# Performance work log

Hardware: AMD Instinct MI355X
Metric: run time of the kernel (lower is better)

Reference implementation:

```python
import jax, jax.numpy as jnp
import numpy as np

BATCH = 256
DIMS = [256, 512, 256, 128]  # input_dim + hidden_dims + [output_dim]
GRID = 5


def _kan_layer(x, w, s, b, g):
    # x: (B, in); w: (out, in, G); s: (out, in); b: (out,); g: (G,)
    xn = jnp.tanh(x)
    # distances: (B, out, in, G)
    d = jnp.abs(xn[:, None, :, None] - g[None, None, None, :])
    basis = jnp.exp(-d * s[None, :, :, None])
    # sum over grid then in_features, fused into one einsum
    return jnp.einsum('boig,oig->bo', basis, w) + b


def setup_inputs() -> dict:
    key = jax.random.key(0)
    ks = jax.random.split(key, 8)
    inp = {'x': jax.random.normal(ks[0], (BATCH, DIMS[0]), dtype=jnp.float32)}
    for i in range(3):
        din, dout = DIMS[i], DIMS[i + 1]
        k1, k2 = jax.random.split(ks[i + 1])
        inp[f'w{i}'] = jax.random.normal(k1, (dout, din, GRID), dtype=jnp.float32)
        inp[f's{i}'] = jax.random.normal(k2, (dout, din), dtype=jnp.float32)
        inp[f'b{i}'] = jnp.zeros((dout,), dtype=jnp.float32)
        inp[f'g{i}'] = jnp.linspace(-1.0, 1.0, GRID, dtype=jnp.float32)
    return inp


def reference(x, w0, s0, b0, g0, w1, s1, b1, g1, w2, s2, b2, g2):
    h = _kan_layer(x, w0, s0, b0, g0)
    h = jax.nn.relu(h)
    h = _kan_layer(h, w1, s1, b1, g1)
    h = jax.nn.relu(h)
    h = _kan_layer(h, w2, s2, b2, g2)
    return jnp.tanh(h)
```

## Files before the change

### kernel.cpp

```cpp
#include <hip/hip_runtime.h>
#include <math.h>

#define BATCH 256
#define D0 256
#define D1 512
#define D2 256
#define D3 128

__device__ float g_xnT0[D0 * BATCH];
__device__ float g_xnT1[D1 * BATCH];
__device__ float g_xnT2[D2 * BATCH];

template <int L> __device__ __forceinline__ float* xnT_ptr() {
    if constexpr (L == 0) return g_xnT0;
    else if constexpr (L == 1) return g_xnT1;
    else return g_xnT2;
}

__device__ __forceinline__ float tanh_f32_cr(float x) {
    return (float)tanh((double)x);
}

__global__ void prep_tanhT(const float* __restrict__ x) {
    int i = threadIdx.x;
    int b = blockIdx.x;
    g_xnT0[i * BATCH + b] = tanh_f32_cr(x[b * D0 + i]);
}

template <int IN, int LU>
__device__ __forceinline__ float sse_chain(const float* __restrict__ xnT,
                                           const float* __restrict__ wr,
                                           const float* __restrict__ sr,
                                           const int b)
{
#pragma clang fp contract(off)
    constexpr int K = IN * 5;
    float acc = 0.f;

#pragma unroll 1
    for (int blk = 0; blk < K; blk += 80) {
        const int ibase = blk / 5;
        float xnv[16], svv[16];
#pragma unroll
        for (int ii = 0; ii < 16; ++ii) {
            xnv[ii] = xnT[(ibase + ii) * BATCH + b];
            svv[ii] = sr[ibase + ii];
        }
        float wvv[20];
#pragma unroll
        for (int jj = 0; jj < 20; ++jj)
            wvv[jj] = wr[blk + 4 * jj + LU];
        __builtin_amdgcn_sched_barrier(0);

#pragma unroll
        for (int q = 0; q < 5; ++q) {
            double uu[4], pp[4];
            int ni[4];
#pragma unroll
            for (int j = 0; j < 4; ++j) {
                constexpr int Uq[4] = {0, 4, 8, 12};
                const int U = q * 16 + Uq[j];
                const int c = U % 5;
                const int sum = c + LU;
                const int carry = (sum >= 5) ? 1 : 0;
                const int idx = U / 5 + carry;
                const float gv = 0.5f * (float)(sum - 5 * carry) - 1.0f;
                const float d = fabsf(xnv[idx] - gv);
                const float m = -(d * svv[idx]);
                const double tt = (double)m * 1.4426950408889634;
                const double nn = rint(tt);
                ni[j] = (int)nn;
                uu[j] = (tt - nn) * 0.6931471805599453;
            }
            __builtin_amdgcn_sched_barrier(0);
#pragma unroll
            for (int j = 0; j < 4; ++j) pp[j] = fma(1.0 / 40320.0, uu[j], 1.0 / 5040.0);
            __builtin_amdgcn_sched_barrier(0);
#pragma unroll
            for (int j = 0; j < 4; ++j) pp[j] = fma(pp[j], uu[j], 1.0 / 720.0);
            __builtin_amdgcn_sched_barrier(0);
#pragma unroll
            for (int j = 0; j < 4; ++j) pp[j] = fma(pp[j], uu[j], 1.0 / 120.0);
            __builtin_amdgcn_sched_barrier(0);
#pragma unroll
            for (int j = 0; j < 4; ++j) pp[j] = fma(pp[j], uu[j], 1.0 / 24.0);
            __builtin_amdgcn_sched_barrier(0);
#pragma unroll
            for (int j = 0; j < 4; ++j) pp[j] = fma(pp[j], uu[j], 1.0 / 6.0);
            __builtin_amdgcn_sched_barrier(0);
#pragma unroll
            for (int j = 0; j < 4; ++j) pp[j] = fma(pp[j], uu[j], 0.5);
            __builtin_amdgcn_sched_barrier(0);
#pragma unroll
            for (int j = 0; j < 4; ++j) pp[j] = fma(pp[j], uu[j], 1.0);
            __builtin_amdgcn_sched_barrier(0);
#pragma unroll
            for (int j = 0; j < 4; ++j) pp[j] = fma(pp[j], uu[j], 1.0);
            __builtin_amdgcn_sched_barrier(0);
            float p[4];
#pragma unroll
            for (int j = 0; j < 4; ++j)
                p[j] = ldexpf((float)pp[j], ni[j]) * wvv[q * 4 + j];
            __builtin_amdgcn_sched_barrier(0);
            acc = p[3] + acc;
            acc = p[2] + acc;
            acc = p[1] + acc;
            acc = p[0] + acc;
        }
    }
    return acc;
}

template <int L, int IN, int OUT, bool FINAL>
__global__ __launch_bounds__(256, 8) void kan_layer(
    const float* __restrict__ w, const float* __restrict__ s,
    const float* __restrict__ bias, float* __restrict__ outf)
{
    const int o = blockIdx.x;
    const int tid = threadIdx.x;
    const int lane = tid & 63;
    const int lu = __builtin_amdgcn_readfirstlane(tid >> 6);
    const int b = blockIdx.y * 64 + lane;
    const float* __restrict__ xnT = xnT_ptr<L>();
    const float* __restrict__ wr = w + (size_t)o * IN * 5;
    const float* __restrict__ sr = s + (size_t)o * IN;

    float acc;
    switch (lu) {
        case 0:  acc = sse_chain<IN, 0>(xnT, wr, sr, b); break;
        case 1:  acc = sse_chain<IN, 1>(xnT, wr, sr, b); break;
        case 2:  acc = sse_chain<IN, 2>(xnT, wr, sr, b); break;
        default: acc = sse_chain<IN, 3>(xnT, wr, sr, b); break;
    }

    __shared__ float lds[4 * 64];
    lds[lu * 64 + lane] = acc;
    __syncthreads();
    if (tid < 64) {
        const float v0 = lds[tid];
        const float v1 = lds[64 + tid];
        const float v2 = lds[128 + tid];
        const float v3 = lds[192 + tid];
        float h = (v0 + v1) + (v2 + v3);
        h = h + bias[o];
        const int bb = blockIdx.y * 64 + tid;
        if constexpr (FINAL) {
            outf[bb * OUT + o] = tanh_f32_cr(h);
        } else {
            xnT_ptr<L + 1>()[o * BATCH + bb] = tanh_f32_cr(fmaxf(h, 0.0f));
        }
    }
}

extern "C" void kernel_launch(void* const* d_in, const int* in_sizes, int n_in,
                              void* d_out, int out_size, void* d_ws, size_t ws_size,
                              hipStream_t stream)
{
    const float* x  = (const float*)d_in[0];
    const float* w0 = (const float*)d_in[1];
    const float* s0 = (const float*)d_in[2];
    const float* b0 = (const float*)d_in[3];
    const float* w1 = (const float*)d_in[5];
    const float* s1 = (const float*)d_in[6];
    const float* b1 = (const float*)d_in[7];
    const float* w2 = (const float*)d_in[9];
    const float* s2 = (const float*)d_in[10];
    const float* b2 = (const float*)d_in[11];
    float* out = (float*)d_out;

    prep_tanhT<<<dim3(BATCH), dim3(D0), 0, stream>>>(x);

    kan_layer<0, D0, D1, false><<<dim3(D1, BATCH / 64), dim3(256), 0, stream>>>(w0, s0, b0, nullptr);
    kan_layer<1, D1, D2, false><<<dim3(D2, BATCH / 64), dim3(256), 0, stream>>>(w1, s1, b1, nullptr);
    kan_layer<2, D2, D3, true ><<<dim3(D3, BATCH / 64), dim3(256), 0, stream>>>(w2, s2, b2, out);
}
```

Baseline: 306.2 us.

## Software-pipeline x/s/w loads with double-buffered registers across 80-element blocks

Splits the inner chunk into a phase function that prefetches the next block's activations, first scale values and first weights into a second register buffer while the current block's exp polynomial runs. The rest of the block's s and w values are loaded at the start of each phase. The idea is to hide global-load latency behind the double-precision FMA chain. The cost is higher register use, so launch bounds drop from 8 to 6 waves per SIMD, which may reduce occupancy.

```diff
diff --git a/kernel.cpp b/kernel.cpp
--- a/kernel.cpp
+++ b/kernel.cpp
@@ -27,6 +27,98 @@
     g_xnT0[i * BATCH + b] = tanh_f32_cr(x[b * D0 + i]);
 }
 
+
+template <int LU>
+__device__ __forceinline__ void sse_phase(
+    float& acc,
+    const float (&xnv)[16], const float (&sv0)[4], const float (&wv0)[4],
+    float (&svt)[12], float (&wvt)[16],
+    float (&nxnv)[16], float (&nsv0)[4], float (&nwv0)[4],
+    const float* __restrict__ xnT, const float* __restrict__ wr,
+    const float* __restrict__ sr, const int b, const int blk, const int nblk)
+{
+#pragma clang fp contract(off)
+    const int ibase = blk / 5;
+    const int nibase = nblk / 5;
+
+#pragma unroll
+    for (int ii = 4; ii < 16; ++ii) svt[ii - 4] = sr[ibase + ii];
+#pragma unroll
+    for (int jj = 4; jj < 20; ++jj) wvt[jj - 4] = wr[blk + 4 * jj + LU];
+    __builtin_amdgcn_sched_barrier(0);
+
+#pragma unroll
+    for (int q = 0; q < 5; ++q) {
+        double uu[4], pp[4];
+        int ni[4];
+#pragma unroll
+        for (int j = 0; j < 4; ++j) {
+            constexpr int Uq[4] = {0, 4, 8, 12};
+            const int U = q * 16 + Uq[j];
+            const int c = U % 5;
+            const int sum = c + LU;
+            const int carry = (sum >= 5) ? 1 : 0;
+            const int idx = U / 5 + carry;
+            const float gv = 0.5f * (float)(sum - 5 * carry) - 1.0f;
+            const float xv = xnv[idx];
+            const float sv = (idx < 4) ? sv0[idx] : svt[idx - 4];
+            const float d = fabsf(xv - gv);
+            const float m = -(d * sv);
+            const double tt = (double)m * 1.4426950408889634;
+            const double nn = rint(tt);
+            ni[j] = (int)nn;
+            uu[j] = (tt - nn) * 0.6931471805599453;
+        }
+        __builtin_amdgcn_sched_barrier(0);
+#pragma unroll
+        for (int j = 0; j < 4; ++j) pp[j] = fma(1.0 / 40320.0, uu[j], 1.0 / 5040.0);
+        __builtin_amdgcn_sched_barrier(0);
+#pragma unroll
+        for (int j = 0; j < 4; ++j) pp[j] = fma(pp[j], uu[j], 1.0 / 720.0);
+        __builtin_amdgcn_sched_barrier(0);
+#pragma unroll
+        for (int j = 0; j < 4; ++j) pp[j] = fma(pp[j], uu[j], 1.0 / 120.0);
+        __builtin_amdgcn_sched_barrier(0);
+#pragma unroll
+        for (int j = 0; j < 4; ++j) pp[j] = fma(pp[j], uu[j], 1.0 / 24.0);
+        __builtin_amdgcn_sched_barrier(0);
+#pragma unroll
+        for (int j = 0; j < 4; ++j) pp[j] = fma(pp[j], uu[j], 1.0 / 6.0);
+        __builtin_amdgcn_sched_barrier(0);
+#pragma unroll
+        for (int j = 0; j < 4; ++j) pp[j] = fma(pp[j], uu[j], 0.5);
+        __builtin_amdgcn_sched_barrier(0);
+#pragma unroll
+        for (int j = 0; j < 4; ++j) pp[j] = fma(pp[j], uu[j], 1.0);
+        __builtin_amdgcn_sched_barrier(0);
+#pragma unroll
+        for (int j = 0; j < 4; ++j) pp[j] = fma(pp[j], uu[j], 1.0);
+        __builtin_amdgcn_sched_barrier(0);
+        float p[4];
+#pragma unroll
+        for (int j = 0; j < 4; ++j) {
+            const int n = q * 4 + j;
+            const float wv = (n < 4) ? wv0[n] : wvt[n - 4];
+            p[j] = ldexpf((float)pp[j], ni[j]) * wv;
+        }
+        __builtin_amdgcn_sched_barrier(0);
+        acc = p[3] + acc;
+        acc = p[2] + acc;
+        acc = p[1] + acc;
+        acc = p[0] + acc;
+
+        if (q == 0) {
+#pragma unroll
+            for (int ii = 0; ii < 16; ++ii)
+                nxnv[ii] = xnT[(nibase + ii) * BATCH + b];
+#pragma unroll
+            for (int ii = 0; ii < 4; ++ii) nsv0[ii] = sr[nibase + ii];
+#pragma unroll
+            for (int jj = 0; jj < 4; ++jj) nwv0[jj] = wr[nblk + 4 * jj + LU];
+        }
+    }
+}
+
 template <int IN, int LU>
 __device__ __forceinline__ float sse_chain(const float* __restrict__ xnT,
                                            const float* __restrict__ wr,
@@ -37,82 +129,31 @@
     constexpr int K = IN * 5;
     float acc = 0.f;
 
+    float xnvA[16], xnvB[16];
+    float svA0[4], svB0[4], wvA0[4], wvB0[4];
+    float svt[12], wvt[16];
+
+#pragma unroll
+    for (int ii = 0; ii < 16; ++ii) xnvA[ii] = xnT[ii * BATCH + b];
+#pragma unroll
+    for (int ii = 0; ii < 4; ++ii) svA0[ii] = sr[ii];
+#pragma unroll
+    for (int jj = 0; jj < 4; ++jj) wvA0[jj] = wr[4 * jj + LU];
+
 #pragma unroll 1
-    for (int blk = 0; blk < K; blk += 80) {
-        const int ibase = blk / 5;
-        float xnv[16], svv[16];
-#pragma unroll
-        for (int ii = 0; ii < 16; ++ii) {
-            xnv[ii] = xnT[(ibase + ii) * BATCH + b];
-            svv[ii] = sr[ibase + ii];
-        }
-        float wvv[20];
-#pragma unroll
-        for (int jj = 0; jj < 20; ++jj)
-            wvv[jj] = wr[blk + 4 * jj + LU];
-        __builtin_amdgcn_sched_barrier(0);
-
-#pragma unroll
-        for (int q = 0; q < 5; ++q) {
-            double uu[4], pp[4];
-            int ni[4];
-#pragma unroll
-            for (int j = 0; j < 4; ++j) {
-                constexpr int Uq[4] = {0, 4, 8, 12};
-                const int U = q * 16 + Uq[j];
-                const int c = U % 5;
-                const int sum = c + LU;
-                const int carry = (sum >= 5) ? 1 : 0;
-                const int idx = U / 5 + carry;
-                const float gv = 0.5f * (float)(sum - 5 * carry) - 1.0f;
-                const float d = fabsf(xnv[idx] - gv);
-                const float m = -(d * svv[idx]);
-                const double tt = (double)m * 1.4426950408889634;
-                const double nn = rint(tt);
-                ni[j] = (int)nn;
-                uu[j] = (tt - nn) * 0.6931471805599453;
-            }
-            __builtin_amdgcn_sched_barrier(0);
-#pragma unroll
-            for (int j = 0; j < 4; ++j) pp[j] = fma(1.0 / 40320.0, uu[j], 1.0 / 5040.0);
-            __builtin_amdgcn_sched_barrier(0);
-#pragma unroll
-            for (int j = 0; j < 4; ++j) pp[j] = fma(pp[j], uu[j], 1.0 / 720.0);
-            __builtin_amdgcn_sched_barrier(0);
-#pragma unroll
-            for (int j = 0; j < 4; ++j) pp[j] = fma(pp[j], uu[j], 1.0 / 120.0);
-            __builtin_amdgcn_sched_barrier(0);
-#pragma unroll
-            for (int j = 0; j < 4; ++j) pp[j] = fma(pp[j], uu[j], 1.0 / 24.0);
-            __builtin_amdgcn_sched_barrier(0);
-#pragma unroll
-            for (int j = 0; j < 4; ++j) pp[j] = fma(pp[j], uu[j], 1.0 / 6.0);
-            __builtin_amdgcn_sched_barrier(0);
-#pragma unroll
-            for (int j = 0; j < 4; ++j) pp[j] = fma(pp[j], uu[j], 0.5);
-            __builtin_amdgcn_sched_barrier(0);
-#pragma unroll
-            for (int j = 0; j < 4; ++j) pp[j] = fma(pp[j], uu[j], 1.0);
-            __builtin_amdgcn_sched_barrier(0);
-#pragma unroll
-            for (int j = 0; j < 4; ++j) pp[j] = fma(pp[j], uu[j], 1.0);
-            __builtin_amdgcn_sched_barrier(0);
-            float p[4];
-#pragma unroll
-            for (int j = 0; j < 4; ++j)
-                p[j] = ldexpf((float)pp[j], ni[j]) * wvv[q * 4 + j];
-            __builtin_amdgcn_sched_barrier(0);
-            acc = p[3] + acc;
-            acc = p[2] + acc;
-            acc = p[1] + acc;
-            acc = p[0] + acc;
-        }
+    for (int blk = 0; blk < K; blk += 160) {
+        const int nb1 = blk + 80;
+        const int nb2 = (blk + 160 < K) ? (blk + 160) : 0;
+        sse_phase<LU>(acc, xnvA, svA0, wvA0, svt, wvt, xnvB, svB0, wvB0,
+                      xnT, wr, sr, b, blk, nb1);
+        sse_phase<LU>(acc, xnvB, svB0, wvB0, svt, wvt, xnvA, svA0, wvA0,
+                      xnT, wr, sr, b, nb1, nb2);
     }
     return acc;
 }
 
 template <int L, int IN, int OUT, bool FINAL>
-__global__ __launch_bounds__(256, 8) void kan_layer(
+__global__ __launch_bounds__(256, 6) void kan_layer(
     const float* __restrict__ w, const float* __restrict__ s,
     const float* __restrict__ bias, float* __restrict__ outf)
 {
```

After: 321.3 us. +4.9%, slower.

## Double-buffer activation loads across unrolled phases to prefetch next block

Applied to the files above, without the earlier changes.

Splits the inner loop into two phases with ping-pong register buffers so the next 16 activations are loaded while the current block's exp chain is computed. This is meant to hide global-load latency behind the double-precision polynomial work. Launch bounds are relaxed from 8 to 6 waves per SIMD to leave room for the extra registers, which trades occupancy for in-thread prefetch.

```diff
diff --git a/kernel.cpp b/kernel.cpp
--- a/kernel.cpp
+++ b/kernel.cpp
@@ -27,6 +27,78 @@
     g_xnT0[i * BATCH + b] = tanh_f32_cr(x[b * D0 + i]);
 }
 
+
+#define SSE_PHASE(CUR, NXT, BLK, NBLK)                                         \
+  {                                                                            \
+    const int ibase  = (BLK) / 5;                                              \
+    const int nibase = (NBLK) / 5;                                             \
+    float svv[16];                                                             \
+    float wvv[20];                                                             \
+    _Pragma("unroll")                                                          \
+    for (int ii = 0; ii < 16; ++ii) svv[ii] = sr[ibase + ii];                  \
+    _Pragma("unroll")                                                          \
+    for (int jj = 0; jj < 20; ++jj) wvv[jj] = wr[(BLK) + 4 * jj + LU];         \
+    _Pragma("unroll")                                                          \
+    for (int ii = 0; ii < 16; ++ii)                                            \
+        NXT[ii] = xnT[(nibase + ii) * BATCH + b];          \
+    __builtin_amdgcn_sched_barrier(0);                                         \
+    _Pragma("unroll")                                                          \
+    for (int q = 0; q < 5; ++q) {              \
+        double uu[4], pp[4];                                                   \
+        int ni[4];                                                             \
+        _Pragma("unroll")                                                      \
+        for (int j = 0; j < 4; ++j) {                                          \
+            constexpr int Uq[4] = {0, 4, 8, 12};                               \
+            const int U = q * 16 + Uq[j];                    \
+            const int c = U % 5;                             \
+            const int sum = c + LU;                          \
+            const int carry = (sum >= 5) ? 1 : 0;                              \
+            const int idx = U / 5 + carry;                   \
+            const float gv = 0.5f * (float)(sum - 5 * carry) - 1.0f;           \
+            const float d = fabsf(CUR[idx] - gv);                    \
+            const float m = -(d * svv[idx]);                         \
+            const double tt = (double)m * 1.4426950408889634;                  \
+            const double nn = rint(tt);                                        \
+            ni[j] = (int)nn;                                                   \
+            uu[j] = (tt - nn) * 0.6931471805599453;                            \
+        }                                                                      \
+        __builtin_amdgcn_sched_barrier(0);                                     \
+        _Pragma("unroll")                                                      \
+        for (int j = 0; j < 4; ++j) pp[j] = fma(1.0 / 40320.0, uu[j], 1.0 / 5040.0); \
+        __builtin_amdgcn_sched_barrier(0);                                     \
+        _Pragma("unroll")                                                      \
+        for (int j = 0; j < 4; ++j) pp[j] = fma(pp[j], uu[j], 1.0 / 720.0);    \
+        __builtin_amdgcn_sched_barrier(0);                                     \
+        _Pragma("unroll")                                                      \
+        for (int j = 0; j < 4; ++j) pp[j] = fma(pp[j], uu[j], 1.0 / 120.0);    \
+        __builtin_amdgcn_sched_barrier(0);                                     \
+        _Pragma("unroll")                                                      \
+        for (int j = 0; j < 4; ++j) pp[j] = fma(pp[j], uu[j], 1.0 / 24.0);     \
+        __builtin_amdgcn_sched_barrier(0);                                     \
+        _Pragma("unroll")                                                      \
+        for (int j = 0; j < 4; ++j) pp[j] = fma(pp[j], uu[j], 1.0 / 6.0);      \
+        __builtin_amdgcn_sched_barrier(0);                                     \
+        _Pragma("unroll")                                                      \
+        for (int j = 0; j < 4; ++j) pp[j] = fma(pp[j], uu[j], 0.5);            \
+        __builtin_amdgcn_sched_barrier(0);                                     \
+        _Pragma("unroll")                                                      \
+        for (int j = 0; j < 4; ++j) pp[j] = fma(pp[j], uu[j], 1.0);            \
+        __builtin_amdgcn_sched_barrier(0);                                     \
+        _Pragma("unroll")                                                      \
+        for (int j = 0; j < 4; ++j) pp[j] = fma(pp[j], uu[j], 1.0);            \
+        __builtin_amdgcn_sched_barrier(0);                                     \
+        float p[4];                                                            \
+        _Pragma("unroll")                                                      \
+        for (int j = 0; j < 4; ++j)                                            \
+            p[j] = ldexpf((float)pp[j], ni[j]) * wvv[q * 4 + j];               \
+        __builtin_amdgcn_sched_barrier(0);                                     \
+        acc = p[3] + acc;                                                      \
+        acc = p[2] + acc;                                                      \
+        acc = p[1] + acc;                                                      \
+        acc = p[0] + acc;                                                      \
+    }                                                                          \
+  }
+
 template <int IN, int LU>
 __device__ __forceinline__ float sse_chain(const float* __restrict__ xnT,
                                            const float* __restrict__ wr,
@@ -36,83 +108,22 @@
 #pragma clang fp contract(off)
     constexpr int K = IN * 5;
     float acc = 0.f;
+    float xA[16], xB[16];
+
+#pragma unroll
+    for (int ii = 0; ii < 16; ++ii) xA[ii] = xnT[ii * BATCH + b];
 
 #pragma unroll 1
-    for (int blk = 0; blk < K; blk += 80) {
-        const int ibase = blk / 5;
-        float xnv[16], svv[16];
-#pragma unroll
-        for (int ii = 0; ii < 16; ++ii) {
-            xnv[ii] = xnT[(ibase + ii) * BATCH + b];
-            svv[ii] = sr[ibase + ii];
-        }
-        float wvv[20];
-#pragma unroll
-        for (int jj = 0; jj < 20; ++jj)
-            wvv[jj] = wr[blk + 4 * jj + LU];
-        __builtin_amdgcn_sched_barrier(0);
-
-#pragma unroll
-        for (int q = 0; q < 5; ++q) {
-            double uu[4], pp[4];
-            int ni[4];
-#pragma unroll
-            for (int j = 0; j < 4; ++j) {
-                constexpr int Uq[4] = {0, 4, 8, 12};
-                const int U = q * 16 + Uq[j];
-                const int c = U % 5;
-                const int sum = c + LU;
-                const int carry = (sum >= 5) ? 1 : 0;
-                const int idx = U / 5 + carry;
-                const float gv = 0.5f * (float)(sum - 5 * carry) - 1.0f;
-                const float d = fabsf(xnv[idx] - gv);
-                const float m = -(d * svv[idx]);
-                const double tt = (double)m * 1.4426950408889634;
-                const double nn = rint(tt);
-                ni[j] = (int)nn;
-                uu[j] = (tt - nn) * 0.6931471805599453;
-            }
-            __builtin_amdgcn_sched_barrier(0);
-#pragma unroll
-            for (int j = 0; j < 4; ++j) pp[j] = fma(1.0 / 40320.0, uu[j], 1.0 / 5040.0);
-            __builtin_amdgcn_sched_barrier(0);
-#pragma unroll
-            for (int j = 0; j < 4; ++j) pp[j] = fma(pp[j], uu[j], 1.0 / 720.0);
-            __builtin_amdgcn_sched_barrier(0);
-#pragma unroll
-            for (int j = 0; j < 4; ++j) pp[j] = fma(pp[j], uu[j], 1.0 / 120.0);
-            __builtin_amdgcn_sched_barrier(0);
-#pragma unroll
-            for (int j = 0; j < 4; ++j) pp[j] = fma(pp[j], uu[j], 1.0 / 24.0);
-            __builtin_amdgcn_sched_barrier(0);
-#pragma unroll
-            for (int j = 0; j < 4; ++j) pp[j] = fma(pp[j], uu[j], 1.0 / 6.0);
-            __builtin_amdgcn_sched_barrier(0);
-#pragma unroll
-            for (int j = 0; j < 4; ++j) pp[j] = fma(pp[j], uu[j], 0.5);
-            __builtin_amdgcn_sched_barrier(0);
-#pragma unroll
-            for (int j = 0; j < 4; ++j) pp[j] = fma(pp[j], uu[j], 1.0);
-            __builtin_amdgcn_sched_barrier(0);
-#pragma unroll
-            for (int j = 0; j < 4; ++j) pp[j] = fma(pp[j], uu[j], 1.0);
-            __builtin_amdgcn_sched_barrier(0);
-            float p[4];
-#pragma unroll
-            for (int j = 0; j < 4; ++j)
-                p[j] = ldexpf((float)pp[j], ni[j]) * wvv[q * 4 + j];
-            __builtin_amdgcn_sched_barrier(0);
-            acc = p[3] + acc;
-            acc = p[2] + acc;
-            acc = p[1] + acc;
-            acc = p[0] + acc;
-        }
+    for (int blk = 0; blk < K; blk += 160) {
+        const int nb2 = (blk + 160 < K) ? (blk + 160) : 0;
+        SSE_PHASE(xA, xB, blk, blk + 80)
+        SSE_PHASE(xB, xA, blk + 80, nb2)
     }
     return acc;
 }
 
 template <int L, int IN, int OUT, bool FINAL>
-__global__ __launch_bounds__(256, 8) void kan_layer(
+__global__ __launch_bounds__(256, 6) void kan_layer(
     const float* __restrict__ w, const float* __restrict__ s,
     const float* __restrict__ bias, float* __restrict__ outf)
 {
```

After: 311.1 us. No clear change (+1.6%).
